# Kernel tuning notes

Measured on AMD Instinct MI355X. Metric: run time of the kernel, lower is better.

The kernel has to match this reference:

```python
import jax, jax.numpy as jnp
import numpy as np

N, E, B = 10000, 160000, 16
IN, H, A, L, OUT = 16, 64, 8, 2, 1
MSG_IN = 2 * (H + 1) + 1   # 131 = concat(x_i, x_j, additional_message_features)
UPD_IN = H + 1 + H         # 129 = concat(x_aug, aggregated message)


def _tp(h, a, W, b):
    # scalar-irreps fully-connected O3 tensor product == bilinear map + bias
    return jnp.einsum('ni,nj,ijk->nk', h, a, W) + b


def setup_inputs() -> dict:
    key = jax.random.key(0)
    ks = jax.random.split(key, 24)
    f32 = jnp.float32
    def rn(k, shape, scale=1.0):
        return jax.random.normal(k, shape, f32) * scale
    def w(k, shape):
        fan = shape[-3] * shape[-2]
        return rn(k, shape, 1.0 / np.sqrt(fan))
    return {
        'x': rn(ks[0], (N, IN)),
        'edge_index': jax.random.randint(ks[1], (2, E), 0, N),
        'edge_attr': rn(ks[2], (E, A)),
        'node_attr': rn(ks[3], (N, A)),
        'additional_message_features': rn(ks[4], (E, 1)),
        'additional_node_features': rn(ks[5], (N, 1)),
        'batch': jnp.sort(jax.random.randint(ks[6], (N,), 0, B)),
        'W_emb': w(ks[7], (IN + 1, A, H)), 'b_emb': jnp.zeros((H,), f32),
        'Wm1': w(ks[8], (L, MSG_IN, A, H)), 'bm1': jnp.zeros((L, H), f32),
        'Wm2': w(ks[9], (L, H, A, H)), 'bm2': jnp.zeros((L, H), f32),
        'Wu1': w(ks[10], (L, UPD_IN, A, H)), 'bu1': jnp.zeros((L, H), f32),
        'Wu2': w(ks[11], (L, H, A, H)), 'bu2': jnp.zeros((L, H), f32),
        'Wp1': w(ks[12], (H, A, H)), 'bp1': jnp.zeros((H,), f32),
        'Wp2': w(ks[13], (H, A, H)), 'bp2': jnp.zeros((H,), f32),
        'Wq1': rn(ks[14], (H, H), 1.0 / np.sqrt(H)), 'bq1': jnp.zeros((H,), f32),
        'Wq2': rn(ks[15], (H, OUT), 1.0 / np.sqrt(H)), 'bq2': jnp.zeros((OUT,), f32),
    }


def _forward(x, edge_attr, node_attr, amf, anf,
             W_emb, b_emb, Wm1, bm1, Wm2, bm2, Wu1, bu1, Wu2, bu2,
             Wp1, bp1, Wp2, bp2, Wq1, bq1, Wq2, bq2, edge_index, batch):
    silu = jax.nn.silu
    src, dst = edge_index[0], edge_index[1]  # source_to_target: aggregate at dst
    n = x.shape[0]
    # embedding: concat additional node features, bilinear TP with node_attr
    h = _tp(jnp.concatenate([x, anf], -1), node_attr, W_emb, b_emb)          # [N,H]
    for l in range(Wm1.shape[0]):  # loop over structurally distinct layers
        h_aug = jnp.concatenate([h, anf], -1)                                # [N,H+1]
        m_in = jnp.concatenate([h_aug[dst], h_aug[src], amf], -1)            # [E,MSG_IN]
        m = silu(_tp(m_in, edge_attr, Wm1[l], bm1[l]))                       # TP + swish gate
        m = silu(_tp(m, edge_attr, Wm2[l], bm2[l]))                          # sg2=True -> gated too
        agg = jax.ops.segment_sum(m, dst, num_segments=n)                    # scatter-add [N,H]
        u = silu(_tp(jnp.concatenate([h_aug, agg], -1), node_attr, Wu1[l], bu1[l]))
        u = _tp(u, node_attr, Wu2[l], bu2[l])                                # no gate on 2nd TP
        h = h + u                                                            # residual, adnid stripped
    # pre-pool MLP (SwishGate TP then plain TP)
    p = silu(_tp(h, node_attr, Wp1, bp1))
    p = _tp(p, node_attr, Wp2, bp2)                                          # [N,POOL=H]
    # global mean pool over graphs
    counts = jax.ops.segment_sum(jnp.ones((n,), p.dtype), batch, num_segments=B)
    g = jax.ops.segment_sum(p, batch, num_segments=B) / jnp.maximum(counts, 1.0)[:, None]
    # post-pool: TP with trivial 1x0e attr == plain linear
    g = silu(g @ Wq1 + bq1)
    return g @ Wq2 + bq2                                                     # [B,OUT]


def reference(x, edge_index, edge_attr, node_attr, additional_message_features,
              additional_node_features, batch, W_emb, b_emb, Wm1, bm1, Wm2, bm2,
              Wu1, bu1, Wu2, bu2, Wp1, bp1, Wp2, bp2, Wq1, bq1, Wq2, bq2):
    return _forward(x, edge_attr, node_attr, additional_message_features,
                    additional_node_features, W_emb, b_emb, Wm1, bm1, Wm2, bm2,
                    Wu1, bu1, Wu2, bu2, Wp1, bp1, Wp2, bp2, Wq1, bq1, Wq2, bq2,
                    edge_index, batch)
```

## Files before the change

### kernel.cpp

```cpp
#include <hip/hip_runtime.h>
#include <hip/hip_bf16.h>
#include <math.h>

constexpr int N = 10000;
constexpr int E = 160000;
constexpr int B = 16;
constexpr int POOL_CHUNKS = 80;
constexpr int MS = 72;
constexpr int HS = 96;

typedef short bf16x8 __attribute__((ext_vector_type(8)));
typedef short bf16x4 __attribute__((ext_vector_type(4)));
typedef float f32x4 __attribute__((ext_vector_type(4)));

__device__ __forceinline__ float silu_f(float x) {
    return x / (1.0f + __expf(-x));
}
__device__ __forceinline__ float bf2f(short s) {
    union { unsigned u; float f; } c; c.u = (unsigned)(unsigned short)s << 16; return c.f;
}

__global__ __launch_bounds__(256) void k_w2(
        const float* __restrict__ Wsrc,
        __hip_bfloat16* __restrict__ Whi, __hip_bfloat16* __restrict__ Wlo) {
    int idx = blockIdx.x * 256 + threadIdx.x;
    int l = idx >> 15;
    int rem = idx & 32767;
    int kk = rem >> 11;
    int nt = (rem >> 9) & 3;
    int c  = (rem >> 5) & 15;
    int q  = (rem >> 3) & 3;
    int j  = rem & 7;
    int i = q * 16 + kk;
    int k = nt * 16 + c;
    float wv = Wsrc[(size_t)l * 32768 + i * 512 + j * 64 + k];
    __hip_bfloat16 hi = __float2bfloat16(wv);
    Whi[idx] = hi;
    Wlo[idx] = __float2bfloat16(wv - __bfloat162float(hi));
}

__global__ __launch_bounds__(256) void k_wu1(
        const float* __restrict__ Wu1,
        __hip_bfloat16* __restrict__ Whi, __hip_bfloat16* __restrict__ Wlo) {
    int idx = blockIdx.x * 256 + threadIdx.x;
    int l = idx / 67584;
    int rem = idx % 67584;
    int kk = rem / 2048;
    int r2 = rem % 2048;
    int nt = (r2 >> 9) & 3;
    int c  = (r2 >> 5) & 15;
    int q  = (r2 >> 3) & 3;
    int j  = r2 & 7;
    int i = q * 33 + kk;
    float wv = (i < 129) ? Wu1[(size_t)l * 129 * 512 + i * 512 + j * 64 + nt * 16 + c] : 0.f;
    __hip_bfloat16 hi = __float2bfloat16(wv);
    Whi[idx] = hi;
    Wlo[idx] = __float2bfloat16(wv - __bfloat162float(hi));
}

__global__ __launch_bounds__(256) void k_wm1z(
        const float* __restrict__ Wm1, __hip_bfloat16* __restrict__ Whi) {
    int idx = blockIdx.x * 256 + threadIdx.x;
    int l = idx / 71680;
    int rem = idx % 71680;
    int kkn = rem >> 9;
    int off = rem & 511;
    int kk = kkn >> 2;
    int nt = kkn & 3;
    int c16 = off >> 5;
    int q = (off >> 3) & 3;
    int j = off & 7;
    int k = nt * 16 + c16;
    int wi = -1;
    if (kk < 17) { int i = q * 17 + kk; if (i <= 64) wi = i; }
    else if (kk < 34) { int s = q * 17 + (kk - 17); if (s <= 64) wi = 65 + s; }
    else { if (q == 0) wi = 130; }
    float wv = (wi >= 0) ? Wm1[((size_t)l * 131 + wi) * 512 + j * 64 + k] : 0.f;
    Whi[idx] = __float2bfloat16(wv);
}

__device__ __forceinline__ void zgemm_stage(
        const __hip_bfloat16* xsrc, int xstride, int kkmax, int Lq,
        int w, int c16, int q, int lofs, const float* naA,
        const __hip_bfloat16* __restrict__ Whi, const __hip_bfloat16* __restrict__ Wlo,
        float (*part_s)[16][64]) {
    f32x4 zero4 = {0.f, 0.f, 0.f, 0.f};
    f32x4 acc[4];
#pragma unroll
    for (int nt = 0; nt < 4; ++nt) acc[nt] = zero4;
    for (int kk = w; kk < kkmax; kk += 4) {
        bf16x8 bh[4], bl[4];
#pragma unroll
        for (int nt = 0; nt < 4; ++nt) {
            int off = (kk * 4 + nt) * 512 + lofs;
            bh[nt] = *(const bf16x8*)(Whi + off);
            bl[nt] = *(const bf16x8*)(Wlo + off);
        }
        float mv = __bfloat162float(xsrc[c16 * xstride + q * Lq + kk]);
        union { bf16x8 v; __hip_bfloat16 hx[8]; } au;
#pragma unroll
        for (int j = 0; j < 8; ++j) au.hx[j] = __float2bfloat16(mv * naA[j]);
#pragma unroll
        for (int nt = 0; nt < 4; ++nt) {
            acc[nt] = __builtin_amdgcn_mfma_f32_16x16x32_bf16(au.v, bh[nt], acc[nt], 0, 0, 0);
            acc[nt] = __builtin_amdgcn_mfma_f32_16x16x32_bf16(au.v, bl[nt], acc[nt], 0, 0, 0);
        }
    }
#pragma unroll
    for (int nt = 0; nt < 4; ++nt)
#pragma unroll
        for (int r = 0; r < 4; ++r) part_s[w][q * 4 + r][nt * 16 + c16] = acc[nt][r];
}

__global__ __launch_bounds__(256) void k_embed_hb(
        const float* __restrict__ x, const float* __restrict__ anf,
        const float* __restrict__ na, const float* __restrict__ W_emb,
        const float* __restrict__ b_emb,
        float* __restrict__ h, __hip_bfloat16* __restrict__ hb, float* __restrict__ agg) {
    __shared__ float xs[16][18];
    __shared__ float na_s[16][8];
    int tid = threadIdx.x, w = tid >> 6, l = tid & 63;
    int n0 = blockIdx.x * 16;
    {
        int r = tid >> 4, c = tid & 15;
        xs[r][c] = x[(size_t)(n0 + r) * 16 + c];
    }
    if (tid < 16) xs[tid][16] = anf[n0 + tid];
    if (tid < 128) na_s[tid >> 3][tid & 7] = na[(size_t)n0 * 8 + tid];
    float4 z4 = {0.f, 0.f, 0.f, 0.f};
    ((float4*)(agg + (size_t)blockIdx.x * 1024))[tid] = z4;
    for (int t = tid; t < 192; t += 256)
        ((float4*)(hb + (size_t)n0 * HS))[t] = z4;
    __syncthreads();
    float acc[4];
#pragma unroll
    for (int t = 0; t < 4; ++t) acc[t] = b_emb[l];
    for (int i = 0; i < 17; ++i) {
#pragma unroll
        for (int j = 0; j < 8; ++j) {
            float wv = W_emb[(i * 8 + j) * 64 + l];
#pragma unroll
            for (int t = 0; t < 4; ++t) {
                int nn = w * 4 + t;
                acc[t] = fmaf(xs[nn][i] * na_s[nn][j], wv, acc[t]);
            }
        }
    }
    int slot = (l / 17) * 24 + l % 17;
#pragma unroll
    for (int t = 0; t < 4; ++t) {
        int n = n0 + w * 4 + t;
        h[(size_t)n * 64 + l] = acc[t];
        hb[(size_t)n * HS + slot] = __float2bfloat16(acc[t]);
    }
    if (tid < 16) hb[(size_t)(n0 + tid) * HS + 85] = __float2bfloat16(xs[tid][16]);
}

__global__ __launch_bounds__(256, 4) void k_edge(
        const int* __restrict__ eidx, const float* __restrict__ ea,
        const float* __restrict__ amf, const __hip_bfloat16* __restrict__ hb,
        const __hip_bfloat16* __restrict__ W1hi, const float* __restrict__ bm1_l,
        const __hip_bfloat16* __restrict__ W2hi,
        const float* __restrict__ bm2_l, float* __restrict__ agg) {
    __shared__ __align__(16) __hip_bfloat16 m_s[128 * MS];
    __shared__ float ea_s[128][9];
    __shared__ float amf_s[128];
    __shared__ int src_s[128], dst_s[128];
    __shared__ float bm1_s[64], bm2_s[64];
    int tid = threadIdx.x;
    int l = tid & 63, w = tid >> 6;
    int e0 = blockIdx.x * 128;
    for (int idx = tid; idx < 128; idx += 256) {
        src_s[idx] = eidx[e0 + idx];
        dst_s[idx] = eidx[E + e0 + idx];
        amf_s[idx] = amf[e0 + idx];
    }
    for (int idx = tid; idx < 1024; idx += 256) ea_s[idx >> 3][idx & 7] = ea[(size_t)e0 * 8 + idx];
    if (tid < 64) { bm1_s[tid] = bm1_l[tid]; bm2_s[tid] = bm2_l[tid]; }
    __syncthreads();

    int c16 = l & 15, q = l >> 4;
    int e0w = w * 32;
    float eaA[2][8];
    float amfA[2];
#pragma unroll
    for (int mt = 0; mt < 2; ++mt) {
#pragma unroll
        for (int j = 0; j < 8; ++j) eaA[mt][j] = ea_s[e0w + mt * 16 + c16][j];
        amfA[mt] = amf_s[e0w + mt * 16 + c16];
    }
    int lofs = (c16 * 4 + q) * 8;
    f32x4 zero4 = {0.f, 0.f, 0.f, 0.f};

    bf16x4 xD[2][5], xS[2][5];
#pragma unroll
    for (int mt = 0; mt < 2; ++mt) {
        const __hip_bfloat16* bd = hb + (size_t)dst_s[e0w + mt * 16 + c16] * HS + q * 24;
        const __hip_bfloat16* bs = hb + (size_t)src_s[e0w + mt * 16 + c16] * HS + q * 24;
#pragma unroll
        for (int t = 0; t < 5; ++t) {
            xD[mt][t] = *(const bf16x4*)(bd + t * 4);
            xS[mt][t] = *(const bf16x4*)(bs + t * 4);
        }
    }

    f32x4 acc1[2][4];
#pragma unroll
    for (int mt = 0; mt < 2; ++mt)
#pragma unroll
        for (int nt = 0; nt < 4; ++nt) acc1[mt][nt] = zero4;
#pragma unroll
    for (int kk = 0; kk < 17; ++kk) {
        bf16x8 bh[4];
#pragma unroll
        for (int nt = 0; nt < 4; ++nt)
            bh[nt] = *(const bf16x8*)(W1hi + (kk * 4 + nt) * 512 + lofs);
#pragma unroll
        for (int mt = 0; mt < 2; ++mt) {
            float xv = bf2f(xD[mt][kk >> 2][kk & 3]);
            union { bf16x8 v; __hip_bfloat16 hx[8]; } au;
#pragma unroll
            for (int j = 0; j < 8; ++j) au.hx[j] = __float2bfloat16(xv * eaA[mt][j]);
#pragma unroll
            for (int nt = 0; nt < 4; ++nt)
                acc1[mt][nt] = __builtin_amdgcn_mfma_f32_16x16x32_bf16(au.v, bh[nt], acc1[mt][nt], 0, 0, 0);
        }
    }
#pragma unroll
    for (int kk = 0; kk < 17; ++kk) {
        bf16x8 bh[4];
#pragma unroll
        for (int nt = 0; nt < 4; ++nt)
            bh[nt] = *(const bf16x8*)(W1hi + ((17 + kk) * 4 + nt) * 512 + lofs);
#pragma unroll
        for (int mt = 0; mt < 2; ++mt) {
            float xv = bf2f(xS[mt][kk >> 2][kk & 3]);
            union { bf16x8 v; __hip_bfloat16 hx[8]; } au;
#pragma unroll
            for (int j = 0; j < 8; ++j) au.hx[j] = __float2bfloat16(xv * eaA[mt][j]);
#pragma unroll
            for (int nt = 0; nt < 4; ++nt)
                acc1[mt][nt] = __builtin_amdgcn_mfma_f32_16x16x32_bf16(au.v, bh[nt], acc1[mt][nt], 0, 0, 0);
        }
    }
    {
        bf16x8 bh[4];
#pragma unroll
        for (int nt = 0; nt < 4; ++nt)
            bh[nt] = *(const bf16x8*)(W1hi + (34 * 4 + nt) * 512 + lofs);
#pragma unroll
        for (int mt = 0; mt < 2; ++mt) {
            float xv = (q == 0) ? amfA[mt] : 0.f;
            union { bf16x8 v; __hip_bfloat16 hx[8]; } au;
#pragma unroll
            for (int j = 0; j < 8; ++j) au.hx[j] = __float2bfloat16(xv * eaA[mt][j]);
#pragma unroll
            for (int nt = 0; nt < 4; ++nt)
                acc1[mt][nt] = __builtin_amdgcn_mfma_f32_16x16x32_bf16(au.v, bh[nt], acc1[mt][nt], 0, 0, 0);
        }
    }
#pragma unroll
    for (int mt = 0; mt < 2; ++mt)
#pragma unroll
        for (int nt = 0; nt < 4; ++nt) {
            int kd = nt * 16 + c16;
            float bias = bm1_s[kd];
#pragma unroll
            for (int r = 0; r < 4; ++r) {
                int e = e0w + mt * 16 + q * 4 + r;
                m_s[e * MS + kd] = __float2bfloat16(silu_f(bias + acc1[mt][nt][r]));
            }
        }

    bf16x4 mR[2][4];
#pragma unroll
    for (int mt = 0; mt < 2; ++mt)
#pragma unroll
        for (int t = 0; t < 4; ++t)
            mR[mt][t] = *(const bf16x4*)&m_s[(e0w + mt * 16 + c16) * MS + q * 16 + t * 4];

    f32x4 acc[2][4];
#pragma unroll
    for (int mt = 0; mt < 2; ++mt)
#pragma unroll
        for (int nt = 0; nt < 4; ++nt) acc[mt][nt] = zero4;
#pragma unroll
    for (int kk = 0; kk < 16; ++kk) {
        bf16x8 bh[4];
#pragma unroll
        for (int nt = 0; nt < 4; ++nt)
            bh[nt] = *(const bf16x8*)(W2hi + (kk * 4 + nt) * 512 + lofs);
#pragma unroll
        for (int mt = 0; mt < 2; ++mt) {
            float mv = bf2f(mR[mt][kk >> 2][kk & 3]);
            union { bf16x8 v; __hip_bfloat16 h[8]; } au;
#pragma unroll
            for (int j = 0; j < 8; ++j) au.h[j] = __float2bfloat16(mv * eaA[mt][j]);
#pragma unroll
            for (int nt = 0; nt < 4; ++nt)
                acc[mt][nt] = __builtin_amdgcn_mfma_f32_16x16x32_bf16(au.v, bh[nt], acc[mt][nt], 0, 0, 0);
        }
    }
#pragma unroll
    for (int mt = 0; mt < 2; ++mt)
#pragma unroll
        for (int nt = 0; nt < 4; ++nt) {
            int kd = nt * 16 + c16;
            float bias = bm2_s[kd];
#pragma unroll
            for (int r = 0; r < 4; ++r) {
                int e = e0w + mt * 16 + q * 4 + r;
                float v = silu_f(bias + acc[mt][nt][r]);
                atomicAdd(&agg[(size_t)dst_s[e] * 64 + kd], v);
            }
        }
}

__global__ __launch_bounds__(256) void k_upd_hb(
        const float* __restrict__ h_in, const float* __restrict__ anf,
        const float* __restrict__ na, const float* __restrict__ agg_in,
        const __hip_bfloat16* __restrict__ W1hi, const __hip_bfloat16* __restrict__ W1lo,
        const float* __restrict__ bu1_l,
        const __hip_bfloat16* __restrict__ W2hi_, const __hip_bfloat16* __restrict__ W2lo_,
        const float* __restrict__ bu2_l,
        float* __restrict__ h, __hip_bfloat16* __restrict__ hb, float* __restrict__ agg) {
    __shared__ __align__(16) __hip_bfloat16 xa_s[16 * 136];
    __shared__ __align__(16) __hip_bfloat16 u1_s[16 * 72];
    __shared__ float part_s[4][16][64];
    int tid = threadIdx.x;
    int w = tid >> 6, l = tid & 63;
    int n0 = blockIdx.x * 16;
    for (int idx = tid; idx < 16 * 132; idx += 256) {
        int r = idx / 132, c = idx % 132;
        int n = n0 + r;
        float v;
        if (c < 64) v = h_in[(size_t)n * 64 + c];
        else if (c == 64) v = anf[n];
        else if (c < 129) v = agg_in[(size_t)n * 64 + (c - 65)];
        else v = 0.f;
        xa_s[r * 136 + c] = __float2bfloat16(v);
    }
    int c16 = l & 15, q = l >> 4;
    float naA[8];
#pragma unroll
    for (int j = 0; j < 8; ++j) naA[j] = na[(size_t)(n0 + c16) * 8 + j];
    __syncthreads();
    float4 z4 = {0.f, 0.f, 0.f, 0.f};
    ((float4*)(agg + (size_t)blockIdx.x * 1024))[tid] = z4;
    for (int t = tid; t < 192; t += 256)
        ((float4*)(hb + (size_t)n0 * HS))[t] = z4;
    int lofs = (c16 * 4 + q) * 8;
    zgemm_stage(xa_s, 136, 33, 33, w, c16, q, lofs, naA, W1hi, W1lo, part_s);
    __syncthreads();
    for (int t = tid; t < 1024; t += 256) {
        int row = t >> 6, col = t & 63;
        float v = part_s[0][row][col] + part_s[1][row][col] + part_s[2][row][col] +
                  part_s[3][row][col] + bu1_l[col];
        u1_s[row * 72 + col] = __float2bfloat16(silu_f(v));
    }
    __syncthreads();
    zgemm_stage(u1_s, 72, 16, 16, w, c16, q, lofs, naA, W2hi_, W2lo_, part_s);
    __syncthreads();
    for (int t = tid; t < 1024; t += 256) {
        int row = t >> 6, col = t & 63;
        float v = part_s[0][row][col] + part_s[1][row][col] + part_s[2][row][col] +
                  part_s[3][row][col] + bu2_l[col];
        int n = n0 + row;
        float hn = h[(size_t)n * 64 + col] + v;
        h[(size_t)n * 64 + col] = hn;
        hb[(size_t)n * HS + (col / 17) * 24 + col % 17] = __float2bfloat16(hn);
    }
    if (tid < 16) hb[(size_t)(n0 + tid) * HS + 85] = __float2bfloat16(anf[n0 + tid]);
}

__global__ __launch_bounds__(256) void k_upd_prepool(
        const float* __restrict__ h_in, const float* __restrict__ anf,
        const float* __restrict__ na, const float* __restrict__ agg_in,
        const __hip_bfloat16* __restrict__ W1hi, const __hip_bfloat16* __restrict__ W1lo,
        const float* __restrict__ bu1_l,
        const __hip_bfloat16* __restrict__ W2hi_, const __hip_bfloat16* __restrict__ W2lo_,
        const float* __restrict__ bu2_l,
        const __hip_bfloat16* __restrict__ Wp1hi, const __hip_bfloat16* __restrict__ Wp1lo,
        const float* __restrict__ bp1,
        const __hip_bfloat16* __restrict__ Wp2hi, const __hip_bfloat16* __restrict__ Wp2lo,
        const float* __restrict__ bp2,
        float* __restrict__ p2) {
    __shared__ __align__(16) __hip_bfloat16 xa_s[16 * 136];
    __shared__ __align__(16) __hip_bfloat16 u1_s[16 * 72];
    __shared__ __align__(16) __hip_bfloat16 x2_s[16 * 72];
    __shared__ float part_s[4][16][64];
    int tid = threadIdx.x;
    int w = tid >> 6, l = tid & 63;
    int n0 = blockIdx.x * 16;
    for (int idx = tid; idx < 16 * 132; idx += 256) {
        int r = idx / 132, c = idx % 132;
        int n = n0 + r;
        float v;
        if (c < 64) v = h_in[(size_t)n * 64 + c];
        else if (c == 64) v = anf[n];
        else if (c < 129) v = agg_in[(size_t)n * 64 + (c - 65)];
        else v = 0.f;
        xa_s[r * 136 + c] = __float2bfloat16(v);
    }
    int c16 = l & 15, q = l >> 4;
    float naA[8];
#pragma unroll
    for (int j = 0; j < 8; ++j) naA[j] = na[(size_t)(n0 + c16) * 8 + j];
    __syncthreads();
    int lofs = (c16 * 4 + q) * 8;
    zgemm_stage(xa_s, 136, 33, 33, w, c16, q, lofs, naA, W1hi, W1lo, part_s);
    __syncthreads();
    for (int t = tid; t < 1024; t += 256) {
        int row = t >> 6, col = t & 63;
        float v = part_s[0][row][col] + part_s[1][row][col] + part_s[2][row][col] +
                  part_s[3][row][col] + bu1_l[col];
        u1_s[row * 72 + col] = __float2bfloat16(silu_f(v));
    }
    __syncthreads();
    zgemm_stage(u1_s, 72, 16, 16, w, c16, q, lofs, naA, W2hi_, W2lo_, part_s);
    __syncthreads();
    for (int t = tid; t < 1024; t += 256) {
        int row = t >> 6, col = t & 63;
        float v = part_s[0][row][col] + part_s[1][row][col] + part_s[2][row][col] +
                  part_s[3][row][col] + bu2_l[col];
        float hn = h_in[(size_t)(n0 + row) * 64 + col] + v;
        x2_s[row * 72 + col] = __float2bfloat16(hn);
    }
    __syncthreads();
    zgemm_stage(x2_s, 72, 16, 16, w, c16, q, lofs, naA, Wp1hi, Wp1lo, part_s);
    __syncthreads();
    for (int t = tid; t < 1024; t += 256) {
        int row = t >> 6, col = t & 63;
        float v = part_s[0][row][col] + part_s[1][row][col] + part_s[2][row][col] +
                  part_s[3][row][col] + bp1[col];
        u1_s[row * 72 + col] = __float2bfloat16(silu_f(v));
    }
    __syncthreads();
    zgemm_stage(u1_s, 72, 16, 16, w, c16, q, lofs, naA, Wp2hi, Wp2lo, part_s);
    __syncthreads();
    for (int t = tid; t < 1024; t += 256) {
        int row = t >> 6, col = t & 63;
        float v = part_s[0][row][col] + part_s[1][row][col] + part_s[2][row][col] +
                  part_s[3][row][col] + bp2[col];
        p2[(size_t)(n0 + row) * 64 + col] = v;
    }
}

__global__ __launch_bounds__(256) void k_pool(
        const float* __restrict__ p2, const int* __restrict__ batch,
        float* __restrict__ partial_p, float* __restrict__ partial_cnt) {
    __shared__ float acc_s[16 * 64];
    __shared__ float cnt_s[16];
    int tid = threadIdx.x;
    for (int idx = tid; idx < 1024; idx += 256) acc_s[idx] = 0.f;
    if (tid < 16) cnt_s[tid] = 0.f;
    __syncthreads();
    int w = tid >> 6, k = tid & 63;
    int base = blockIdx.x * 125;
    for (int i = 0; i < 32; ++i) {
        int nl = i * 4 + w;
        if (nl < 125) {
            int n = base + nl;
            int b = batch[n];
            atomicAdd(&acc_s[b * 64 + k], p2[(size_t)n * 64 + k]);
            if (k == 0) atomicAdd(&cnt_s[b], 1.0f);
        }
    }
    __syncthreads();
    for (int idx = tid; idx < 1024; idx += 256)
        partial_p[(size_t)blockIdx.x * 1024 + idx] = acc_s[idx];
    if (tid < 16) partial_cnt[blockIdx.x * 16 + tid] = cnt_s[tid];
}

__global__ __launch_bounds__(1024) void k_final(
        const float* __restrict__ partial_p, const float* __restrict__ partial_cnt,
        const float* __restrict__ Wq1, const float* __restrict__ bq1,
        const float* __restrict__ Wq2, const float* __restrict__ bq2,
        float* __restrict__ out) {
    __shared__ float g[16][64];
    int b = threadIdx.x >> 6, k = threadIdx.x & 63;
    float s = 0.f, cc = 0.f;
    for (int c = 0; c < POOL_CHUNKS; ++c) s += partial_p[(size_t)c * 1024 + b * 64 + k];
    for (int c = 0; c < POOL_CHUNKS; ++c) cc += partial_cnt[c * 16 + b];
    g[b][k] = s / fmaxf(cc, 1.0f);
    __syncthreads();
    float acc = bq1[k];
#pragma unroll
    for (int i = 0; i < 64; ++i) acc = fmaf(g[b][i], Wq1[i * 64 + k], acc);
    float v = silu_f(acc) * Wq2[k];
#pragma unroll
    for (int off = 32; off > 0; off >>= 1) v += __shfl_down(v, off, 64);
    if (k == 0) out[b] = v + bq2[0];
}

extern "C" void kernel_launch(void* const* d_in, const int* in_sizes, int n_in,
                              void* d_out, int out_size, void* d_ws, size_t ws_size,
                              hipStream_t stream) {
    const float* x    = (const float*)d_in[0];
    const int*   eidx = (const int*)  d_in[1];
    const float* ea   = (const float*)d_in[2];
    const float* na   = (const float*)d_in[3];
    const float* amf  = (const float*)d_in[4];
    const float* anf  = (const float*)d_in[5];
    const int*   batch= (const int*)  d_in[6];
    const float* W_emb= (const float*)d_in[7];
    const float* b_emb= (const float*)d_in[8];
    const float* Wm1  = (const float*)d_in[9];
    const float* bm1  = (const float*)d_in[10];
    const float* Wm2  = (const float*)d_in[11];
    const float* bm2  = (const float*)d_in[12];
    const float* Wu1  = (const float*)d_in[13];
    const float* bu1  = (const float*)d_in[14];
    const float* Wu2  = (const float*)d_in[15];
    const float* bu2  = (const float*)d_in[16];
    const float* Wp1  = (const float*)d_in[17];
    const float* bp1  = (const float*)d_in[18];
    const float* Wp2  = (const float*)d_in[19];
    const float* bp2  = (const float*)d_in[20];
    const float* Wq1  = (const float*)d_in[21];
    const float* bq1  = (const float*)d_in[22];
    const float* Wq2  = (const float*)d_in[23];
    const float* bq2  = (const float*)d_in[24];

    float* ws = (float*)d_ws;
    float* h      = ws;
    float* agg    = h + (size_t)N * 64;
    float* p2     = agg + (size_t)N * 64;
    float* part_p = p2 + (size_t)N * 64;
    float* part_c = part_p + POOL_CHUNKS * 1024;
    float* fend   = part_c + POOL_CHUNKS * 16;
    __hip_bfloat16* hb     = (__hip_bfloat16*)fend;
    __hip_bfloat16* W2hi   = hb + (size_t)N * HS;
    __hip_bfloat16* W2lo   = W2hi + 65536;
    __hip_bfloat16* Wu2hi  = W2lo + 65536;
    __hip_bfloat16* Wu2lo  = Wu2hi + 65536;
    __hip_bfloat16* Wp1hi  = Wu2lo + 65536;
    __hip_bfloat16* Wp1lo  = Wp1hi + 32768;
    __hip_bfloat16* Wp2hi  = Wp1lo + 32768;
    __hip_bfloat16* Wp2lo  = Wp2hi + 32768;
    __hip_bfloat16* Wu1hi  = Wp2lo + 32768;
    __hip_bfloat16* Wu1lo  = Wu1hi + 135168;
    __hip_bfloat16* Wm1zhi = Wu1lo + 135168;

    k_w2<<<256, 256, 0, stream>>>(Wm2, W2hi, W2lo);
    k_w2<<<256, 256, 0, stream>>>(Wu2, Wu2hi, Wu2lo);
    k_w2<<<128, 256, 0, stream>>>(Wp1, Wp1hi, Wp1lo);
    k_w2<<<128, 256, 0, stream>>>(Wp2, Wp2hi, Wp2lo);
    k_wu1<<<528, 256, 0, stream>>>(Wu1, Wu1hi, Wu1lo);
    k_wm1z<<<560, 256, 0, stream>>>(Wm1, Wm1zhi);

    k_embed_hb<<<625, 256, 0, stream>>>(x, anf, na, W_emb, b_emb, h, hb, agg);
    k_edge<<<E / 128, 256, 0, stream>>>(eidx, ea, amf, hb,
                                        Wm1zhi, bm1, W2hi, bm2, agg);
    k_upd_hb<<<625, 256, 0, stream>>>(h, anf, na, agg,
                                      Wu1hi, Wu1lo, bu1,
                                      Wu2hi, Wu2lo, bu2,
                                      h, hb, agg);
    k_edge<<<E / 128, 256, 0, stream>>>(eidx, ea, amf, hb,
                                        Wm1zhi + 71680, bm1 + 64,
                                        W2hi + 32768, bm2 + 64, agg);
    k_upd_prepool<<<625, 256, 0, stream>>>(h, anf, na, agg,
                                           Wu1hi + 67584, Wu1lo + 67584, bu1 + 64,
                                           Wu2hi + 32768, Wu2lo + 32768, bu2 + 64,
                                           Wp1hi, Wp1lo, bp1, Wp2hi, Wp2lo, bp2, p2);
    k_pool<<<POOL_CHUNKS, 256, 0, stream>>>(p2, batch, part_p, part_c);
    k_final<<<1, 1024, 0, stream>>>(part_p, part_c, Wq1, bq1, Wq2, bq2, (float*)d_out);
}
```

Measured before the change: 384.8 us.

## Fuse weight reorder kernels, fold pooling into prepool kernel, parallelize final

New measurement: 443.8 us. 1.15x slower.

```diff
diff --git a/kernel.cpp b/kernel.cpp
--- a/kernel.cpp
+++ b/kernel.cpp
@@ -5,7 +5,7 @@
 constexpr int N = 10000;
 constexpr int E = 160000;
 constexpr int B = 16;
-constexpr int POOL_CHUNKS = 80;
+constexpr int PC = 625;
 constexpr int MS = 72;
 constexpr int HS = 96;
 
@@ -20,47 +20,27 @@
     union { unsigned u; float f; } c; c.u = (unsigned)(unsigned short)s << 16; return c.f;
 }
 
-__global__ __launch_bounds__(256) void k_w2(
-        const float* __restrict__ Wsrc,
-        __hip_bfloat16* __restrict__ Whi, __hip_bfloat16* __restrict__ Wlo) {
-    int idx = blockIdx.x * 256 + threadIdx.x;
+__device__ __forceinline__ void hilo_store(float wv, __hip_bfloat16* hi, __hip_bfloat16* lo, int idx) {
+    __hip_bfloat16 hh = __float2bfloat16(wv);
+    hi[idx] = hh;
+    lo[idx] = __float2bfloat16(wv - __bfloat162float(hh));
+}
+__device__ __forceinline__ float zr64q(const float* __restrict__ W, int idx) {
     int l = idx >> 15;
     int rem = idx & 32767;
-    int kk = rem >> 11;
-    int nt = (rem >> 9) & 3;
-    int c  = (rem >> 5) & 15;
-    int q  = (rem >> 3) & 3;
-    int j  = rem & 7;
-    int i = q * 16 + kk;
-    int k = nt * 16 + c;
-    float wv = Wsrc[(size_t)l * 32768 + i * 512 + j * 64 + k];
-    __hip_bfloat16 hi = __float2bfloat16(wv);
-    Whi[idx] = hi;
-    Wlo[idx] = __float2bfloat16(wv - __bfloat162float(hi));
-}
-
-__global__ __launch_bounds__(256) void k_wu1(
-        const float* __restrict__ Wu1,
-        __hip_bfloat16* __restrict__ Whi, __hip_bfloat16* __restrict__ Wlo) {
-    int idx = blockIdx.x * 256 + threadIdx.x;
+    int kk = rem >> 11, nt = (rem >> 9) & 3, c = (rem >> 5) & 15, q = (rem >> 3) & 3, j = rem & 7;
+    return W[(size_t)l * 32768 + (size_t)(q * 16 + kk) * 512 + j * 64 + nt * 16 + c];
+}
+__device__ __forceinline__ float wu1q(const float* __restrict__ W, int idx) {
     int l = idx / 67584;
     int rem = idx % 67584;
     int kk = rem / 2048;
     int r2 = rem % 2048;
-    int nt = (r2 >> 9) & 3;
-    int c  = (r2 >> 5) & 15;
-    int q  = (r2 >> 3) & 3;
-    int j  = r2 & 7;
+    int nt = (r2 >> 9) & 3, c = (r2 >> 5) & 15, q = (r2 >> 3) & 3, j = r2 & 7;
     int i = q * 33 + kk;
-    float wv = (i < 129) ? Wu1[(size_t)l * 129 * 512 + i * 512 + j * 64 + nt * 16 + c] : 0.f;
-    __hip_bfloat16 hi = __float2bfloat16(wv);
-    Whi[idx] = hi;
-    Wlo[idx] = __float2bfloat16(wv - __bfloat162float(hi));
-}
-
-__global__ __launch_bounds__(256) void k_wm1z(
-        const float* __restrict__ Wm1, __hip_bfloat16* __restrict__ Whi) {
-    int idx = blockIdx.x * 256 + threadIdx.x;
+    return (i < 129) ? W[(size_t)l * 129 * 512 + (size_t)i * 512 + j * 64 + nt * 16 + c] : 0.f;
+}
+__device__ __forceinline__ float wm1zq(const float* __restrict__ W, int idx) {
     int l = idx / 71680;
     int rem = idx % 71680;
     int kkn = rem >> 9;
@@ -75,8 +55,24 @@
     if (kk < 17) { int i = q * 17 + kk; if (i <= 64) wi = i; }
     else if (kk < 34) { int s = q * 17 + (kk - 17); if (s <= 64) wi = 65 + s; }
     else { if (q == 0) wi = 130; }
-    float wv = (wi >= 0) ? Wm1[((size_t)l * 131 + wi) * 512 + j * 64 + k] : 0.f;
-    Whi[idx] = __float2bfloat16(wv);
+    return (wi >= 0) ? W[((size_t)l * 131 + wi) * 512 + j * 64 + k] : 0.f;
+}
+__global__ __launch_bounds__(256) void k_reorder(
+        const float* __restrict__ Wm2, const float* __restrict__ Wm1,
+        const float* __restrict__ Wu1, const float* __restrict__ Wu2,
+        const float* __restrict__ Wp1, const float* __restrict__ Wp2,
+        __hip_bfloat16* W2hi, __hip_bfloat16* Wm1zhi,
+        __hip_bfloat16* Wu1hi, __hip_bfloat16* Wu1lo,
+        __hip_bfloat16* Wu2hi, __hip_bfloat16* Wu2lo,
+        __hip_bfloat16* Wp1hi, __hip_bfloat16* Wp1lo,
+        __hip_bfloat16* Wp2hi, __hip_bfloat16* Wp2lo) {
+    int idx = blockIdx.x * 256 + threadIdx.x;
+    if (idx < 65536)        W2hi[idx] = __float2bfloat16(zr64q(Wm2, idx));
+    else if (idx < 208896) { int i2 = idx - 65536;  Wm1zhi[i2] = __float2bfloat16(wm1zq(Wm1, i2)); }
+    else if (idx < 344064) { int i2 = idx - 208896; hilo_store(wu1q(Wu1, i2), Wu1hi, Wu1lo, i2); }
+    else if (idx < 409600) { int i2 = idx - 344064; hilo_store(zr64q(Wu2, i2), Wu2hi, Wu2lo, i2); }
+    else if (idx < 442368) { int i2 = idx - 409600; hilo_store(zr64q(Wp1, i2), Wp1hi, Wp1lo, i2); }
+    else if (idx < 475136) { int i2 = idx - 442368; hilo_store(zr64q(Wp2, i2), Wp2hi, Wp2lo, i2); }
 }
 
 __device__ __forceinline__ void zgemm_stage(
@@ -376,6 +372,7 @@
 __global__ __launch_bounds__(256) void k_upd_prepool(
         const float* __restrict__ h_in, const float* __restrict__ anf,
         const float* __restrict__ na, const float* __restrict__ agg_in,
+        const int* __restrict__ batch,
         const __hip_bfloat16* __restrict__ W1hi, const __hip_bfloat16* __restrict__ W1lo,
         const float* __restrict__ bu1_l,
         const __hip_bfloat16* __restrict__ W2hi_, const __hip_bfloat16* __restrict__ W2lo_,
@@ -384,14 +381,19 @@
         const float* __restrict__ bp1,
         const __hip_bfloat16* __restrict__ Wp2hi, const __hip_bfloat16* __restrict__ Wp2lo,
         const float* __restrict__ bp2,
-        float* __restrict__ p2) {
+        float* __restrict__ partial_p, float* __restrict__ partial_cnt) {
     __shared__ __align__(16) __hip_bfloat16 xa_s[16 * 136];
     __shared__ __align__(16) __hip_bfloat16 u1_s[16 * 72];
     __shared__ __align__(16) __hip_bfloat16 x2_s[16 * 72];
     __shared__ float part_s[4][16][64];
+    __shared__ float pool_s[16][64];
+    __shared__ float cnt_s[16];
+    __shared__ int batch_s[16];
     int tid = threadIdx.x;
     int w = tid >> 6, l = tid & 63;
     int n0 = blockIdx.x * 16;
+    for (int idx = tid; idx < 1024; idx += 256) pool_s[idx >> 6][idx & 63] = 0.f;
+    if (tid < 16) { cnt_s[tid] = 0.f; batch_s[tid] = batch[n0 + tid]; }
     for (int idx = tid; idx < 16 * 132; idx += 256) {
         int r = idx / 132, c = idx % 132;
         int n = n0 + r;
@@ -407,6 +409,7 @@
 #pragma unroll
     for (int j = 0; j < 8; ++j) naA[j] = na[(size_t)(n0 + c16) * 8 + j];
     __syncthreads();
+    if (tid < 16) atomicAdd(&cnt_s[batch_s[tid]], 1.0f);
     int lofs = (c16 * 4 + q) * 8;
     zgemm_stage(xa_s, 136, 33, 33, w, c16, q, lofs, naA, W1hi, W1lo, part_s);
     __syncthreads();
@@ -442,55 +445,48 @@
         int row = t >> 6, col = t & 63;
         float v = part_s[0][row][col] + part_s[1][row][col] + part_s[2][row][col] +
                   part_s[3][row][col] + bp2[col];
-        p2[(size_t)(n0 + row) * 64 + col] = v;
-    }
-}
-
-__global__ __launch_bounds__(256) void k_pool(
-        const float* __restrict__ p2, const int* __restrict__ batch,
-        float* __restrict__ partial_p, float* __restrict__ partial_cnt) {
-    __shared__ float acc_s[16 * 64];
-    __shared__ float cnt_s[16];
-    int tid = threadIdx.x;
-    for (int idx = tid; idx < 1024; idx += 256) acc_s[idx] = 0.f;
-    if (tid < 16) cnt_s[tid] = 0.f;
-    __syncthreads();
-    int w = tid >> 6, k = tid & 63;
-    int base = blockIdx.x * 125;
-    for (int i = 0; i < 32; ++i) {
-        int nl = i * 4 + w;
-        if (nl < 125) {
-            int n = base + nl;
-            int b = batch[n];
-            atomicAdd(&acc_s[b * 64 + k], p2[(size_t)n * 64 + k]);
-            if (k == 0) atomicAdd(&cnt_s[b], 1.0f);
-        }
-    }
-    __syncthreads();
-    for (int idx = tid; idx < 1024; idx += 256)
-        partial_p[(size_t)blockIdx.x * 1024 + idx] = acc_s[idx];
+        atomicAdd(&pool_s[batch_s[row]][col], v);
+    }
+    __syncthreads();
+    for (int t = tid; t < 1024; t += 256)
+        partial_p[(size_t)blockIdx.x * 1024 + t] = pool_s[t >> 6][t & 63];
     if (tid < 16) partial_cnt[blockIdx.x * 16 + tid] = cnt_s[tid];
 }
 
-__global__ __launch_bounds__(1024) void k_final(
+__global__ __launch_bounds__(256) void k_final(
         const float* __restrict__ partial_p, const float* __restrict__ partial_cnt,
         const float* __restrict__ Wq1, const float* __restrict__ bq1,
         const float* __restrict__ Wq2, const float* __restrict__ bq2,
         float* __restrict__ out) {
-    __shared__ float g[16][64];
-    int b = threadIdx.x >> 6, k = threadIdx.x & 63;
-    float s = 0.f, cc = 0.f;
-    for (int c = 0; c < POOL_CHUNKS; ++c) s += partial_p[(size_t)c * 1024 + b * 64 + k];
-    for (int c = 0; c < POOL_CHUNKS; ++c) cc += partial_cnt[c * 16 + b];
-    g[b][k] = s / fmaxf(cc, 1.0f);
-    __syncthreads();
-    float acc = bq1[k];
-#pragma unroll
-    for (int i = 0; i < 64; ++i) acc = fmaf(g[b][i], Wq1[i * 64 + k], acc);
-    float v = silu_f(acc) * Wq2[k];
-#pragma unroll
-    for (int off = 32; off > 0; off >>= 1) v += __shfl_down(v, off, 64);
-    if (k == 0) out[b] = v + bq2[0];
+    __shared__ float red[4][64];
+    __shared__ float cred[4];
+    __shared__ float g_s[64];
+    int b = blockIdx.x;
+    int tid = threadIdx.x;
+    int k = tid & 63, part = tid >> 6;
+    float s = 0.f;
+    for (int c = part; c < PC; c += 4) s += partial_p[(size_t)c * 1024 + b * 64 + k];
+    red[part][k] = s;
+    if (k == 0) {
+        float cc = 0.f;
+        for (int c = part; c < PC; c += 4) cc += partial_cnt[c * 16 + b];
+        cred[part] = cc;
+    }
+    __syncthreads();
+    if (tid < 64) {
+        float cnt = cred[0] + cred[1] + cred[2] + cred[3];
+        g_s[k] = (red[0][k] + red[1][k] + red[2][k] + red[3][k]) / fmaxf(cnt, 1.0f);
+    }
+    __syncthreads();
+    if (tid < 64) {
+        float acc = bq1[k];
+#pragma unroll
+        for (int i = 0; i < 64; ++i) acc = fmaf(g_s[i], Wq1[i * 64 + k], acc);
+        float v = silu_f(acc) * Wq2[k];
+#pragma unroll
+        for (int off = 32; off > 0; off >>= 1) v += __shfl_down(v, off, 64);
+        if (k == 0) out[b] = v + bq2[0];
+    }
 }
 
 extern "C" void kernel_launch(void* const* d_in, const int* in_sizes, int n_in,
@@ -525,29 +521,24 @@
     float* ws = (float*)d_ws;
     float* h      = ws;
     float* agg    = h + (size_t)N * 64;
-    float* p2     = agg + (size_t)N * 64;
-    float* part_p = p2 + (size_t)N * 64;
-    float* part_c = part_p + POOL_CHUNKS * 1024;
-    float* fend   = part_c + POOL_CHUNKS * 16;
+    float* part_p = agg + (size_t)N * 64;
+    float* part_c = part_p + (size_t)PC * 1024;
+    float* fend   = part_c + PC * 16;
     __hip_bfloat16* hb     = (__hip_bfloat16*)fend;
     __hip_bfloat16* W2hi   = hb + (size_t)N * HS;
-    __hip_bfloat16* W2lo   = W2hi + 65536;
-    __hip_bfloat16* Wu2hi  = W2lo + 65536;
+    __hip_bfloat16* Wm1zhi = W2hi + 65536;
+    __hip_bfloat16* Wu1hi  = Wm1zhi + 143360;
+    __hip_bfloat16* Wu1lo  = Wu1hi + 135168;
+    __hip_bfloat16* Wu2hi  = Wu1lo + 135168;
     __hip_bfloat16* Wu2lo  = Wu2hi + 65536;
     __hip_bfloat16* Wp1hi  = Wu2lo + 65536;
     __hip_bfloat16* Wp1lo  = Wp1hi + 32768;
     __hip_bfloat16* Wp2hi  = Wp1lo + 32768;
     __hip_bfloat16* Wp2lo  = Wp2hi + 32768;
-    __hip_bfloat16* Wu1hi  = Wp2lo + 32768;
-    __hip_bfloat16* Wu1lo  = Wu1hi + 135168;
-    __hip_bfloat16* Wm1zhi = Wu1lo + 135168;
-
-    k_w2<<<256, 256, 0, stream>>>(Wm2, W2hi, W2lo);
-    k_w2<<<256, 256, 0, stream>>>(Wu2, Wu2hi, Wu2lo);
-    k_w2<<<128, 256, 0, stream>>>(Wp1, Wp1hi, Wp1lo);
-    k_w2<<<128, 256, 0, stream>>>(Wp2, Wp2hi, Wp2lo);
-    k_wu1<<<528, 256, 0, stream>>>(Wu1, Wu1hi, Wu1lo);
-    k_wm1z<<<560, 256, 0, stream>>>(Wm1, Wm1zhi);
+
+    k_reorder<<<1856, 256, 0, stream>>>(Wm2, Wm1, Wu1, Wu2, Wp1, Wp2,
+                                        W2hi, Wm1zhi, Wu1hi, Wu1lo,
+                                        Wu2hi, Wu2lo, Wp1hi, Wp1lo, Wp2hi, Wp2lo);
 
     k_embed_hb<<<625, 256, 0, stream>>>(x, anf, na, W_emb, b_emb, h, hb, agg);
     k_edge<<<E / 128, 256, 0, stream>>>(eidx, ea, amf, hb,
@@ -559,10 +550,10 @@
     k_edge<<<E / 128, 256, 0, stream>>>(eidx, ea, amf, hb,
                                         Wm1zhi + 71680, bm1 + 64,
                                         W2hi + 32768, bm2 + 64, agg);
-    k_upd_prepool<<<625, 256, 0, stream>>>(h, anf, na, agg,
+    k_upd_prepool<<<625, 256, 0, stream>>>(h, anf, na, agg, batch,
                                            Wu1hi + 67584, Wu1lo + 67584, bu1 + 64,
                                            Wu2hi + 32768, Wu2lo + 32768, bu2 + 64,
-                                           Wp1hi, Wp1lo, bp1, Wp2hi, Wp2lo, bp2, p2);
-    k_pool<<<POOL_CHUNKS, 256, 0, stream>>>(p2, batch, part_p, part_c);
-    k_final<<<1, 1024, 0, stream>>>(part_p, part_c, Wq1, bq1, Wq2, bq2, (float*)d_out);
-}
+                                           Wp1hi, Wp1lo, bp1, Wp2hi, Wp2lo, bp2,
+                                           part_p, part_c);
+    k_final<<<B, 256, 0, stream>>>(part_p, part_c, Wq1, bq1, Wq2, bq2, (float*)d_out);
+}
```
